# Kernel tuning notes

Hardware: AMD Instinct MI355X
Metric: run time of the kernel (lower is better)

## Reference

```python
import jax, jax.numpy as jnp
import numpy as np

N, E, G = 10000, 40000, 128          # nodes, edges, graphs
NF, EF, H, NH, GD, L = 92, 50, 64, 10, 108, 5  # feat dims, hidden, heads, global dim, layers
EPS = 1e-5

def _lrelu(v):
    return jax.nn.leaky_relu(v, 0.2)

def setup_inputs() -> dict:
    key = jax.random.key(0)
    ks = jax.random.split(key, 24)
    def rn(k, shp, s=0.05):
        return jax.random.normal(k, shp, jnp.float32) * s
    return {
        "x": jax.random.normal(ks[0], (N, NF), jnp.float32),
        "edge_index": jax.random.randint(ks[1], (2, E), 0, N, dtype=jnp.int32),
        "edge_attr": jax.random.normal(ks[2], (E, EF), jnp.float32),
        "batch_idx": jnp.sort(jax.random.randint(ks[3], (N,), 0, G, dtype=jnp.int32)),
        "global_features": jax.random.normal(ks[4], (G, GD), jnp.float32),
        "node_W": rn(ks[5], (NF, H)), "node_b": jnp.zeros((H,), jnp.float32),
        "edge_W": rn(ks[6], (EF, H)), "edge_b": jnp.zeros((H,), jnp.float32),
        "conv_W": rn(ks[7], (L, 2 * H, NH * H)),
        "conv_att": rn(ks[8], (L, NH, 2 * H)),
        "conv_b": jnp.zeros((L, H), jnp.float32),
        "conv_gamma": jnp.ones((L, NH), jnp.float32),
        "conv_beta": jnp.zeros((L, NH), jnp.float32),
        "ga_W1": rn(ks[9], (H + GD, H)), "ga_b1": jnp.zeros((H,), jnp.float32),
        "ga_W2": rn(ks[10], (H, 1)), "ga_b2": jnp.zeros((1,), jnp.float32),
        "out_W1": rn(ks[11], (H, H)), "out_b1": jnp.zeros((H,), jnp.float32),
        "out_W2": rn(ks[12], (H, 1)), "out_b2": jnp.zeros((1,), jnp.float32),
    }

def reference(x, edge_index, edge_attr, batch_idx, global_features,
              node_W, node_b, edge_W, edge_b,
              conv_W, conv_att, conv_b, conv_gamma, conv_beta,
              ga_W1, ga_b1, ga_W2, ga_b2, out_W1, out_b1, out_W2, out_b2):
    row, col = edge_index[0], edge_index[1]
    # embeddings
    h = _lrelu(x @ node_W + node_b)            # [N, H]
    ea = _lrelu(edge_attr @ edge_W + edge_b)   # [E, H]
    initial = h
    inv_std = 1.0 / jnp.sqrt(1.0 + EPS)        # DiffGroupNorm eval: running mean=0, var=1
    for i in range(L):
        xi = jnp.concatenate([h[row], ea], axis=-1)               # [E, 2H]
        xj = jnp.concatenate([h[col], ea], axis=-1)
        hi = _lrelu(xi @ conv_W[i]).reshape(E, NH, H)             # [E, NH, H]
        hj = _lrelu(xj @ conv_W[i]).reshape(E, NH, H)
        alpha = jnp.sum(jnp.concatenate([hi, hj], -1) * conv_att[i][None], -1)  # [E, NH]
        alpha = _lrelu(alpha)
        alpha = alpha * inv_std * conv_gamma[i] + conv_beta[i]
        alpha = jax.nn.softmax(alpha, axis=1)                     # softmax over heads
        msg = (hj * alpha[..., None]).reshape(E, NH * H)
        agg = jax.ops.segment_sum(msg, row, num_segments=N).reshape(N, NH, H)
        h_new = agg.mean(axis=1) + conv_b[i]
        h = h + h_new if i > 0 else h_new
    h = h + initial
    # global attention: softmax over nodes within each graph
    g = global_features[batch_idx]                                 # [N, GD]
    s = _lrelu(jnp.concatenate([h, g], -1) @ ga_W1 + ga_b1)
    score = (s @ ga_W2 + ga_b2)[:, 0]                              # [N]
    smax = jax.ops.segment_max(score, batch_idx, num_segments=G)
    ex = jnp.exp(score - smax[batch_idx])
    denom = jax.ops.segment_sum(ex, batch_idx, num_segments=G)
    w = (ex / denom[batch_idx])[:, None]
    h = h * w
    pooled = jax.ops.segment_sum(h, batch_idx, num_segments=G)     # [G, H]
    out = jax.nn.relu(pooled @ out_W1 + out_b1) @ out_W2 + out_b2
    return out[:, 0]
```

## Files before the change

kernel.cpp:

```cpp
#include <hip/hip_runtime.h>
#include <hip/hip_bf16.h>

#define LRELU(v) ((v) > 0.f ? (v) : 0.2f * (v))

__global__ __launch_bounds__(256) void embed_kernel(
    const float* __restrict__ X, const float* __restrict__ W,
    const float* __restrict__ b, float* __restrict__ out, int M, int K) {
  const int lane = threadIdx.x & 63;
  const int r =
      __builtin_amdgcn_readfirstlane(blockIdx.x * 4 + (threadIdx.x >> 6));
  if (r >= M) return;
  float acc = b[lane];
  const float* Xr = X + (size_t)r * K;
  const float* Wl = W + lane;
  for (int k = 0; k < K; ++k) acc = fmaf(Xr[k], Wl[(size_t)k * 64], acc);
  acc = LRELU(acc);
  out[(size_t)r * 64 + lane] = acc;
}

template <int ROWS>
__global__ __launch_bounds__(256) void gemm_k64_kernel(
    const float* __restrict__ A, const float* __restrict__ W,
    float* __restrict__ C, int M) {
  const int lane = threadIdx.x & 63;
  const int wv =
      __builtin_amdgcn_readfirstlane(blockIdx.x * 4 + (threadIdx.x >> 6));
  const int r0 = wv * ROWS;
  if (r0 >= M) return;
  float acc[ROWS][10];
#pragma unroll
  for (int r = 0; r < ROWS; ++r)
#pragma unroll
    for (int h = 0; h < 10; ++h) acc[r][h] = 0.f;
  const float* Arow = A + (size_t)r0 * 64;
  const float* Wl = W + lane;
  for (int k = 0; k < 64; ++k) {
    float w[10];
#pragma unroll
    for (int h = 0; h < 10; ++h) w[h] = Wl[(size_t)k * 640 + h * 64];
#pragma unroll
    for (int r = 0; r < ROWS; ++r) {
      float a = Arow[r * 64 + k];
#pragma unroll
      for (int h = 0; h < 10; ++h) acc[r][h] = fmaf(a, w[h], acc[r][h]);
    }
  }
#pragma unroll
  for (int r = 0; r < ROWS; ++r) {
    float* Crow = C + (size_t)(r0 + r) * 640;
#pragma unroll
    for (int h = 0; h < 10; ++h) Crow[h * 64 + lane] = acc[r][h];
  }
}

__global__ __launch_bounds__(256) void edge_fused_kernel(
    const float* __restrict__ P, const float* __restrict__ ea,
    const float* __restrict__ Wbot,
    const int* __restrict__ row, const int* __restrict__ col,
    const float* __restrict__ att, const float* __restrict__ gamma,
    const float* __restrict__ beta, float* __restrict__ agg, int E_) {
  const int lane = threadIdx.x & 63;
  const int wv =
      __builtin_amdgcn_readfirstlane(blockIdx.x * 4 + (threadIdx.x >> 6));
  const int e0 = wv * 8;
  if (e0 >= E_) return;

  int eix[8], ris[8], cis[8];
#pragma unroll
  for (int r = 0; r < 8; ++r) {
    int e = (e0 + r < E_) ? (e0 + r) : (E_ - 1);
    eix[r] = e;
    ris[r] = row[e];
    cis[r] = col[e];
  }

  float qacc[8][10];
#pragma unroll
  for (int r = 0; r < 8; ++r)
#pragma unroll
    for (int h = 0; h < 10; ++h) qacc[r][h] = 0.f;

  const float* Wl = Wbot + lane;
  for (int k = 0; k < 64; ++k) {
    float w[10];
#pragma unroll
    for (int h = 0; h < 10; ++h) w[h] = Wl[k * 640 + h * 64];
#pragma unroll
    for (int r = 0; r < 8; ++r) {
      float a = ea[(size_t)eix[r] * 64 + k];
#pragma unroll
      for (int h = 0; h < 10; ++h) qacc[r][h] = fmaf(a, w[h], qacc[r][h]);
    }
  }

  const float inv_std = 0.9999950000374997f;

  float prb[10], pcb[10];
  {
    const float* Pr = P + (size_t)ris[0] * 640 + lane;
    const float* Pc = P + (size_t)cis[0] * 640 + lane;
#pragma unroll
    for (int h = 0; h < 10; ++h) {
      prb[h] = Pr[h * 64];
      pcb[h] = Pc[h * 64];
    }
  }

#pragma unroll
  for (int r = 0; r < 8; ++r) {
    int e = e0 + r;
    if (e >= E_) break;
    float pr[10], pc[10];
#pragma unroll
    for (int h = 0; h < 10; ++h) {
      pr[h] = prb[h];
      pc[h] = pcb[h];
    }
    if (r + 1 < 8) {
      const float* Pr = P + (size_t)ris[r + 1] * 640 + lane;
      const float* Pc = P + (size_t)cis[r + 1] * 640 + lane;
#pragma unroll
      for (int h = 0; h < 10; ++h) {
        prb[h] = Pr[h * 64];
        pcb[h] = Pc[h * 64];
      }
    }
    float hj[10], val[10];
#pragma unroll
    for (int h = 0; h < 10; ++h) {
      float q = qacc[r][h];
      float hi = pr[h] + q;
      float hjv = pc[h] + q;
      hi = LRELU(hi);
      hjv = LRELU(hjv);
      hj[h] = hjv;
      val[h] = fmaf(hi, att[h * 128 + lane], hjv * att[h * 128 + 64 + lane]);
    }
#pragma unroll
    for (int h = 0; h < 10; ++h) {
      float v = val[h];
#pragma unroll
      for (int off = 32; off; off >>= 1) v += __shfl_xor(v, off);
      val[h] = v;
    }
    float mx = -1e30f;
#pragma unroll
    for (int h = 0; h < 10; ++h) {
      float a = val[h];
      a = LRELU(a);
      a = fmaf(a * inv_std, gamma[h], beta[h]);
      val[h] = a;
      mx = fmaxf(mx, a);
    }
    float ssum = 0.f;
#pragma unroll
    for (int h = 0; h < 10; ++h) {
      float ex = __expf(val[h] - mx);
      val[h] = ex;
      ssum += ex;
    }
    float inv = 1.0f / ssum;
    float m = 0.f;
#pragma unroll
    for (int h = 0; h < 10; ++h) m = fmaf(val[h] * inv, hj[h], m);
    atomicAdd(agg + (size_t)ris[r] * 64 + lane, m);
  }
}

__global__ __launch_bounds__(256) void finalize_kernel(
    float* __restrict__ h, float* __restrict__ agg, const float* __restrict__ b,
    const float* __restrict__ h0, int mode, int total) {
  int idx = blockIdx.x * 256 + threadIdx.x;
  if (idx >= total) return;
  int f = idx & 63;
  float v = fmaf(agg[idx], 0.1f, b[f]);
  agg[idx] = 0.f;
  if (mode >= 1) v += h[idx];
  if (mode == 2) v += h0[idx];
  h[idx] = v;
}

__global__ __launch_bounds__(256) void score_kernel(
    const float* __restrict__ h, const int* __restrict__ batch,
    const float* __restrict__ gf, const float* __restrict__ W1,
    const float* __restrict__ b1, const float* __restrict__ W2,
    const float* __restrict__ b2, float* __restrict__ score, int N_) {
  const int lane = threadIdx.x & 63;
  const int n =
      __builtin_amdgcn_readfirstlane(blockIdx.x * 4 + (threadIdx.x >> 6));
  if (n >= N_) return;
  float acc = b1[lane];
  const float* hn = h + (size_t)n * 64;
  const float* W1l = W1 + lane;
#pragma unroll 8
  for (int k = 0; k < 64; ++k) acc = fmaf(hn[k], W1l[k * 64], acc);
  const int bn = batch[n];
  const float* g = gf + (size_t)bn * 108;
#pragma unroll 4
  for (int k = 0; k < 108; ++k) acc = fmaf(g[k], W1l[(64 + k) * 64], acc);
  acc = LRELU(acc);
  float v = acc * W2[lane];
#pragma unroll
  for (int off = 32; off; off >>= 1) v += __shfl_xor(v, off);
  if (lane == 0) score[n] = v + b2[0];
}

__global__ void bounds_kernel(const int* __restrict__ batch,
                              int* __restrict__ start, int N_, int G_) {
  int n = blockIdx.x * blockDim.x + threadIdx.x;
  if (n >= N_) return;
  int b = batch[n];
  int bp = (n == 0) ? -1 : batch[n - 1];
  for (int g = bp + 1; g <= b; ++g) start[g] = n;
  if (n == N_ - 1)
    for (int g = b + 1; g <= G_; ++g) start[g] = N_;
}

__global__ __launch_bounds__(256) void pool_out_kernel(
    const float* __restrict__ h, const float* __restrict__ score,
    const int* __restrict__ start, const float* __restrict__ W1,
    const float* __restrict__ b1, const float* __restrict__ W2,
    const float* __restrict__ b2, float* __restrict__ out) {
  int g = blockIdx.x;
  int s0 = start[g], s1 = start[g + 1];
  int tid = threadIdx.x;
  __shared__ float red[256];
  __shared__ float pool[64];
  __shared__ float sh_smax, sh_denom;
  float lm = -1e30f;
  for (int n = s0 + tid; n < s1; n += 256) lm = fmaxf(lm, score[n]);
  red[tid] = lm;
  __syncthreads();
  for (int off = 128; off; off >>= 1) {
    if (tid < off) red[tid] = fmaxf(red[tid], red[tid + off]);
    __syncthreads();
  }
  if (tid == 0) sh_smax = red[0];
  __syncthreads();
  float smax = sh_smax;
  __syncthreads();
  float ls = 0.f;
  for (int n = s0 + tid; n < s1; n += 256) ls += __expf(score[n] - smax);
  red[tid] = ls;
  __syncthreads();
  for (int off = 128; off; off >>= 1) {
    if (tid < off) red[tid] += red[tid + off];
    __syncthreads();
  }
  if (tid == 0) sh_denom = red[0];
  __syncthreads();
  float denom = sh_denom;
  float invd = denom > 0.f ? 1.0f / denom : 0.f;
  __syncthreads();
  int f = tid & 63, sub = tid >> 6;
  float acc = 0.f;
  for (int n = s0 + sub; n < s1; n += 4)
    acc = fmaf(__expf(score[n] - smax), h[(size_t)n * 64 + f], acc);
  red[tid] = acc;
  __syncthreads();
  if (tid < 64)
    pool[tid] =
        (red[tid] + red[tid + 64] + red[tid + 128] + red[tid + 192]) * invd;
  __syncthreads();
  if (tid < 64) {
    float a = b1[tid];
#pragma unroll 8
    for (int k = 0; k < 64; ++k) a = fmaf(pool[k], W1[k * 64 + tid], a);
    a = fmaxf(a, 0.f);
    red[tid] = a * W2[tid];
  }
  __syncthreads();
  if (tid == 0) {
    float s = 0.f;
    for (int k = 0; k < 64; ++k) s += red[k];
    out[g] = s + b2[0];
  }
}

extern "C" void kernel_launch(void* const* d_in, const int* in_sizes, int n_in,
                              void* d_out, int out_size, void* d_ws,
                              size_t ws_size, hipStream_t stream) {
  const float* x          = (const float*)d_in[0];
  const int*   edge_index = (const int*)d_in[1];
  const float* edge_attr  = (const float*)d_in[2];
  const int*   batch_idx  = (const int*)d_in[3];
  const float* gf         = (const float*)d_in[4];
  const float* node_W     = (const float*)d_in[5];
  const float* node_b     = (const float*)d_in[6];
  const float* edge_W     = (const float*)d_in[7];
  const float* edge_b     = (const float*)d_in[8];
  const float* conv_W     = (const float*)d_in[9];
  const float* conv_att   = (const float*)d_in[10];
  const float* conv_b     = (const float*)d_in[11];
  const float* conv_gamma = (const float*)d_in[12];
  const float* conv_beta  = (const float*)d_in[13];
  const float* ga_W1      = (const float*)d_in[14];
  const float* ga_b1      = (const float*)d_in[15];
  const float* ga_W2      = (const float*)d_in[16];
  const float* ga_b2      = (const float*)d_in[17];
  const float* out_W1     = (const float*)d_in[18];
  const float* out_b1     = (const float*)d_in[19];
  const float* out_W2     = (const float*)d_in[20];
  const float* out_b2     = (const float*)d_in[21];
  float* out = (float*)d_out;

  const int N = in_sizes[3];
  const int E = in_sizes[2] / 50;
  const int G = in_sizes[4] / 108;
  const int L = 5;

  float* ws = (float*)d_ws;
  float* h    = ws;  ws += (size_t)N * 64;
  float* h0   = ws;  ws += (size_t)N * 64;
  float* ea   = ws;  ws += (size_t)E * 64;
  float* P    = ws;  ws += (size_t)N * 640;
  float* agg  = ws;  ws += (size_t)N * 64;
  float* scr  = ws;  ws += N;
  int* gstart = (int*)ws;

  const int* row = edge_index;
  const int* col = edge_index + E;

  embed_kernel<<<(N + 3) / 4, 256, 0, stream>>>(x, node_W, node_b, h0, N, 92);
  embed_kernel<<<(E + 3) / 4, 256, 0, stream>>>(edge_attr, edge_W, edge_b, ea,
                                                E, 50);
  hipMemsetAsync(agg, 0, (size_t)N * 64 * sizeof(float), stream);

  for (int i = 0; i < L; ++i) {
    const float* Wi = conv_W + (size_t)i * 128 * 640;
    gemm_k64_kernel<4><<<(N / 4 + 3) / 4, 256, 0, stream>>>(i == 0 ? h0 : h,
                                                            Wi, P, N);
    int waves = (E + 7) / 8;
    edge_fused_kernel<<<(waves + 3) / 4, 256, 0, stream>>>(
        P, ea, Wi + 64 * 640, row, col, conv_att + (size_t)i * 1280,
        conv_gamma + i * 10, conv_beta + i * 10, agg, E);
    int mode = (i == 0) ? 0 : (i == L - 1 ? 2 : 1);
    finalize_kernel<<<(N * 64 + 255) / 256, 256, 0, stream>>>(
        h, agg, conv_b + i * 64, h0, mode, N * 64);
  }

  score_kernel<<<(N + 3) / 4, 256, 0, stream>>>(h, batch_idx, gf, ga_W1, ga_b1,
                                                ga_W2, ga_b2, scr, N);
  bounds_kernel<<<(N + 255) / 256, 256, 0, stream>>>(batch_idx, gstart, N, G);
  pool_out_kernel<<<G, 256, 0, stream>>>(h, scr, gstart, out_W1, out_b1, out_W2,
                                         out_b2, out);
}
```

Baseline: 780.4 us.

## Fuse finalize into node GEMM, merge embeddings, use DPP wave reductions

Merges the two embedding launches into one kernel. It folds each layer's finalize step (bias, residual, zeroing agg) into the next layer's node GEMM, so only one finalize remains after the loop. The GEMM now takes its A operand from registers through lane shuffles, and both GEMM loops double-buffer the weight loads. Wave reductions use DPP row operations instead of xor shuffles, and occupancy hints are added via launch_bounds. The aim is fewer launches and less global traffic and shuffle latency, at the cost of added register pressure and code complexity.

```diff
diff --git a/kernel.cpp b/kernel.cpp
--- a/kernel.cpp
+++ b/kernel.cpp
@@ -1,14 +1,42 @@
 #include <hip/hip_runtime.h>
-#include <hip/hip_bf16.h>
 
 #define LRELU(v) ((v) > 0.f ? (v) : 0.2f * (v))
 
-__global__ __launch_bounds__(256) void embed_kernel(
-    const float* __restrict__ X, const float* __restrict__ W,
-    const float* __restrict__ b, float* __restrict__ out, int M, int K) {
+template <int CTRL, int RMASK>
+__device__ __forceinline__ float dpp_add(float v) {
+  int moved = __builtin_amdgcn_update_dpp(0, __builtin_bit_cast(int, v), CTRL,
+                                          RMASK, 0xf, true);
+  return v + __builtin_bit_cast(float, moved);
+}
+__device__ __forceinline__ float wave_sum(float v) {
+  v = dpp_add<0x111, 0xf>(v);
+  v = dpp_add<0x112, 0xf>(v);
+  v = dpp_add<0x114, 0xf>(v);
+  v = dpp_add<0x118, 0xf>(v);
+  v = dpp_add<0x142, 0xa>(v);
+  v = dpp_add<0x143, 0xc>(v);
+  return __builtin_bit_cast(
+      float, __builtin_amdgcn_readlane(__builtin_bit_cast(int, v), 63));
+}
+
+__global__ __launch_bounds__(256) void embed2_kernel(
+    const float* __restrict__ x, const float* __restrict__ nW,
+    const float* __restrict__ nb, float* __restrict__ h0, int N_,
+    const float* __restrict__ eattr, const float* __restrict__ eW,
+    const float* __restrict__ eb, float* __restrict__ ea, int E_,
+    int nodeBlocks) {
   const int lane = threadIdx.x & 63;
-  const int r =
-      __builtin_amdgcn_readfirstlane(blockIdx.x * 4 + (threadIdx.x >> 6));
+  const float *X, *W, *b;
+  float* out;
+  int M, K, r;
+  if ((int)blockIdx.x < nodeBlocks) {
+    r = blockIdx.x * 4 + (threadIdx.x >> 6);
+    X = x; W = nW; b = nb; out = h0; M = N_; K = 92;
+  } else {
+    r = (blockIdx.x - nodeBlocks) * 4 + (threadIdx.x >> 6);
+    X = eattr; W = eW; b = eb; out = ea; M = E_; K = 50;
+  }
+  r = __builtin_amdgcn_readfirstlane(r);
   if (r >= M) return;
   float acc = b[lane];
   const float* Xr = X + (size_t)r * K;
@@ -18,42 +46,70 @@
   out[(size_t)r * 64 + lane] = acc;
 }
 
-template <int ROWS>
-__global__ __launch_bounds__(256) void gemm_k64_kernel(
-    const float* __restrict__ A, const float* __restrict__ W,
-    float* __restrict__ C, int M) {
+__global__ __launch_bounds__(256, 4) void update_gemm_kernel(
+    const float* __restrict__ A0, float* __restrict__ h,
+    float* __restrict__ agg, const float* __restrict__ bvec,
+    const float* __restrict__ W, float* __restrict__ P, int M, int mode) {
   const int lane = threadIdx.x & 63;
   const int wv =
       __builtin_amdgcn_readfirstlane(blockIdx.x * 4 + (threadIdx.x >> 6));
-  const int r0 = wv * ROWS;
+  const int r0 = wv * 4;
   if (r0 >= M) return;
-  float acc[ROWS][10];
-#pragma unroll
-  for (int r = 0; r < ROWS; ++r)
-#pragma unroll
-    for (int h = 0; h < 10; ++h) acc[r][h] = 0.f;
-  const float* Arow = A + (size_t)r0 * 64;
+  float hv[4];
+  if (mode < 0) {
+#pragma unroll
+    for (int r = 0; r < 4; ++r) hv[r] = A0[(size_t)(r0 + r) * 64 + lane];
+  } else {
+    float bl = bvec[lane];
+#pragma unroll
+    for (int r = 0; r < 4; ++r) {
+      size_t idx = (size_t)(r0 + r) * 64 + lane;
+      float v = fmaf(agg[idx], 0.1f, bl);
+      if (mode >= 1) v += h[idx];
+      agg[idx] = 0.f;
+      h[idx] = v;
+      hv[r] = v;
+    }
+  }
+  float acc[4][10];
+#pragma unroll
+  for (int r = 0; r < 4; ++r)
+#pragma unroll
+    for (int q = 0; q < 10; ++q) acc[r][q] = 0.f;
   const float* Wl = W + lane;
-  for (int k = 0; k < 64; ++k) {
-    float w[10];
-#pragma unroll
-    for (int h = 0; h < 10; ++h) w[h] = Wl[(size_t)k * 640 + h * 64];
-#pragma unroll
-    for (int r = 0; r < ROWS; ++r) {
-      float a = Arow[r * 64 + k];
-#pragma unroll
-      for (int h = 0; h < 10; ++h) acc[r][h] = fmaf(a, w[h], acc[r][h]);
-    }
-  }
-#pragma unroll
-  for (int r = 0; r < ROWS; ++r) {
-    float* Crow = C + (size_t)(r0 + r) * 640;
-#pragma unroll
-    for (int h = 0; h < 10; ++h) Crow[h * 64 + lane] = acc[r][h];
-  }
-}
-
-__global__ __launch_bounds__(256) void edge_fused_kernel(
+  float wa[10], wb[10];
+#pragma unroll
+  for (int q = 0; q < 10; ++q) wa[q] = Wl[q * 64];
+#pragma unroll 1
+  for (int k = 0; k < 64; k += 2) {
+#pragma unroll
+    for (int q = 0; q < 10; ++q) wb[q] = Wl[(k + 1) * 640 + q * 64];
+#pragma unroll
+    for (int r = 0; r < 4; ++r) {
+      float a = __shfl(hv[r], k);
+#pragma unroll
+      for (int q = 0; q < 10; ++q) acc[r][q] = fmaf(a, wa[q], acc[r][q]);
+    }
+    if (k + 2 < 64) {
+#pragma unroll
+      for (int q = 0; q < 10; ++q) wa[q] = Wl[(k + 2) * 640 + q * 64];
+    }
+#pragma unroll
+    for (int r = 0; r < 4; ++r) {
+      float a = __shfl(hv[r], k + 1);
+#pragma unroll
+      for (int q = 0; q < 10; ++q) acc[r][q] = fmaf(a, wb[q], acc[r][q]);
+    }
+  }
+#pragma unroll
+  for (int r = 0; r < 4; ++r) {
+    float* Crow = P + (size_t)(r0 + r) * 640;
+#pragma unroll
+    for (int q = 0; q < 10; ++q) Crow[q * 64 + lane] = acc[r][q];
+  }
+}
+
+__global__ __launch_bounds__(256, 3) void edge_fused_kernel(
     const float* __restrict__ P, const float* __restrict__ ea,
     const float* __restrict__ Wbot,
     const int* __restrict__ row, const int* __restrict__ col,
@@ -78,106 +134,117 @@
 #pragma unroll
   for (int r = 0; r < 8; ++r)
 #pragma unroll
-    for (int h = 0; h < 10; ++h) qacc[r][h] = 0.f;
+    for (int q = 0; q < 10; ++q) qacc[r][q] = 0.f;
 
   const float* Wl = Wbot + lane;
-  for (int k = 0; k < 64; ++k) {
-    float w[10];
-#pragma unroll
-    for (int h = 0; h < 10; ++h) w[h] = Wl[k * 640 + h * 64];
+  float wa[10], wb[10];
+#pragma unroll
+  for (int q = 0; q < 10; ++q) wa[q] = Wl[q * 64];
+#pragma unroll 1
+  for (int k = 0; k < 64; k += 2) {
+#pragma unroll
+    for (int q = 0; q < 10; ++q) wb[q] = Wl[(k + 1) * 640 + q * 64];
 #pragma unroll
     for (int r = 0; r < 8; ++r) {
       float a = ea[(size_t)eix[r] * 64 + k];
 #pragma unroll
-      for (int h = 0; h < 10; ++h) qacc[r][h] = fmaf(a, w[h], qacc[r][h]);
+      for (int q = 0; q < 10; ++q) qacc[r][q] = fmaf(a, wa[q], qacc[r][q]);
+    }
+    if (k + 2 < 64) {
+#pragma unroll
+      for (int q = 0; q < 10; ++q) wa[q] = Wl[(k + 2) * 640 + q * 64];
+    }
+#pragma unroll
+    for (int r = 0; r < 8; ++r) {
+      float a = ea[(size_t)eix[r] * 64 + k + 1];
+#pragma unroll
+      for (int q = 0; q < 10; ++q) qacc[r][q] = fmaf(a, wb[q], qacc[r][q]);
     }
   }
 
   const float inv_std = 0.9999950000374997f;
+  float gm[10], bt[10];
+#pragma unroll
+  for (int q = 0; q < 10; ++q) {
+    gm[q] = gamma[q];
+    bt[q] = beta[q];
+  }
 
   float prb[10], pcb[10];
   {
     const float* Pr = P + (size_t)ris[0] * 640 + lane;
     const float* Pc = P + (size_t)cis[0] * 640 + lane;
 #pragma unroll
-    for (int h = 0; h < 10; ++h) {
-      prb[h] = Pr[h * 64];
-      pcb[h] = Pc[h * 64];
+    for (int q = 0; q < 10; ++q) {
+      prb[q] = Pr[q * 64];
+      pcb[q] = Pc[q * 64];
     }
   }
 
 #pragma unroll
   for (int r = 0; r < 8; ++r) {
-    int e = e0 + r;
-    if (e >= E_) break;
+    if (e0 + r >= E_) break;
     float pr[10], pc[10];
 #pragma unroll
-    for (int h = 0; h < 10; ++h) {
-      pr[h] = prb[h];
-      pc[h] = pcb[h];
+    for (int q = 0; q < 10; ++q) {
+      pr[q] = prb[q];
+      pc[q] = pcb[q];
     }
     if (r + 1 < 8) {
       const float* Pr = P + (size_t)ris[r + 1] * 640 + lane;
       const float* Pc = P + (size_t)cis[r + 1] * 640 + lane;
 #pragma unroll
-      for (int h = 0; h < 10; ++h) {
-        prb[h] = Pr[h * 64];
-        pcb[h] = Pc[h * 64];
+      for (int q = 0; q < 10; ++q) {
+        prb[q] = Pr[q * 64];
+        pcb[q] = Pc[q * 64];
       }
     }
-    float hj[10], val[10];
-#pragma unroll
-    for (int h = 0; h < 10; ++h) {
-      float q = qacc[r][h];
-      float hi = pr[h] + q;
-      float hjv = pc[h] + q;
+    float hj[10], sv[10];
+#pragma unroll
+    for (int q = 0; q < 10; ++q) {
+      float qc = qacc[r][q];
+      float hi = pr[q] + qc;
+      float hjv = pc[q] + qc;
       hi = LRELU(hi);
       hjv = LRELU(hjv);
-      hj[h] = hjv;
-      val[h] = fmaf(hi, att[h * 128 + lane], hjv * att[h * 128 + 64 + lane]);
-    }
-#pragma unroll
-    for (int h = 0; h < 10; ++h) {
-      float v = val[h];
-#pragma unroll
-      for (int off = 32; off; off >>= 1) v += __shfl_xor(v, off);
-      val[h] = v;
+      hj[q] = hjv;
+      float part =
+          fmaf(hi, att[q * 128 + lane], hjv * att[q * 128 + 64 + lane]);
+      sv[q] = wave_sum(part);
     }
     float mx = -1e30f;
 #pragma unroll
-    for (int h = 0; h < 10; ++h) {
-      float a = val[h];
+    for (int q = 0; q < 10; ++q) {
+      float a = sv[q];
       a = LRELU(a);
-      a = fmaf(a * inv_std, gamma[h], beta[h]);
-      val[h] = a;
+      a = fmaf(a * inv_std, gm[q], bt[q]);
+      sv[q] = a;
       mx = fmaxf(mx, a);
     }
     float ssum = 0.f;
 #pragma unroll
-    for (int h = 0; h < 10; ++h) {
-      float ex = __expf(val[h] - mx);
-      val[h] = ex;
+    for (int q = 0; q < 10; ++q) {
+      float ex = __expf(sv[q] - mx);
+      sv[q] = ex;
       ssum += ex;
     }
     float inv = 1.0f / ssum;
     float m = 0.f;
 #pragma unroll
-    for (int h = 0; h < 10; ++h) m = fmaf(val[h] * inv, hj[h], m);
+    for (int q = 0; q < 10; ++q) m = fmaf(sv[q] * inv, hj[q], m);
     atomicAdd(agg + (size_t)ris[r] * 64 + lane, m);
   }
 }
 
 __global__ __launch_bounds__(256) void finalize_kernel(
     float* __restrict__ h, float* __restrict__ agg, const float* __restrict__ b,
-    const float* __restrict__ h0, int mode, int total) {
+    const float* __restrict__ h0, int total) {
   int idx = blockIdx.x * 256 + threadIdx.x;
   if (idx >= total) return;
   int f = idx & 63;
   float v = fmaf(agg[idx], 0.1f, b[f]);
   agg[idx] = 0.f;
-  if (mode >= 1) v += h[idx];
-  if (mode == 2) v += h0[idx];
-  h[idx] = v;
+  h[idx] = v + h[idx] + h0[idx];
 }
 
 __global__ __launch_bounds__(256) void score_kernel(
@@ -199,9 +266,7 @@
 #pragma unroll 4
   for (int k = 0; k < 108; ++k) acc = fmaf(g[k], W1l[(64 + k) * 64], acc);
   acc = LRELU(acc);
-  float v = acc * W2[lane];
-#pragma unroll
-  for (int off = 32; off; off >>= 1) v += __shfl_xor(v, off);
+  float v = wave_sum(acc * W2[lane]);
   if (lane == 0) score[n] = v + b2[0];
 }
 
@@ -321,23 +386,29 @@
   const int* row = edge_index;
   const int* col = edge_index + E;
 
-  embed_kernel<<<(N + 3) / 4, 256, 0, stream>>>(x, node_W, node_b, h0, N, 92);
-  embed_kernel<<<(E + 3) / 4, 256, 0, stream>>>(edge_attr, edge_W, edge_b, ea,
-                                                E, 50);
-  hipMemsetAsync(agg, 0, (size_t)N * 64 * sizeof(float), stream);
+  int nodeBlocks = (N + 3) / 4;
+  int edgeBlocks = (E + 3) / 4;
+  embed2_kernel<<<nodeBlocks + edgeBlocks, 256, 0, stream>>>(
+      x, node_W, node_b, h0, N, edge_attr, edge_W, edge_b, ea, E, nodeBlocks);
+  (void)hipMemsetAsync(agg, 0, (size_t)N * 64 * sizeof(float), stream);
 
   for (int i = 0; i < L; ++i) {
     const float* Wi = conv_W + (size_t)i * 128 * 640;
-    gemm_k64_kernel<4><<<(N / 4 + 3) / 4, 256, 0, stream>>>(i == 0 ? h0 : h,
-                                                            Wi, P, N);
+    if (i == 0) {
+      update_gemm_kernel<<<(N / 4 + 3) / 4, 256, 0, stream>>>(
+          h0, h, agg, nullptr, Wi, P, N, -1);
+    } else {
+      update_gemm_kernel<<<(N / 4 + 3) / 4, 256, 0, stream>>>(
+          nullptr, h, agg, conv_b + (i - 1) * 64, Wi, P, N,
+          (i - 1) == 0 ? 0 : 1);
+    }
     int waves = (E + 7) / 8;
     edge_fused_kernel<<<(waves + 3) / 4, 256, 0, stream>>>(
         P, ea, Wi + 64 * 640, row, col, conv_att + (size_t)i * 1280,
         conv_gamma + i * 10, conv_beta + i * 10, agg, E);
-    int mode = (i == 0) ? 0 : (i == L - 1 ? 2 : 1);
-    finalize_kernel<<<(N * 64 + 255) / 256, 256, 0, stream>>>(
-        h, agg, conv_b + i * 64, h0, mode, N * 64);
-  }
+  }
+  finalize_kernel<<<(N * 64 + 255) / 256, 256, 0, stream>>>(
+      h, agg, conv_b + (L - 1) * 64, h0, N * 64);
 
   score_kernel<<<(N + 3) / 4, 256, 0, stream>>>(h, batch_idx, gf, ga_W1, ga_b1,
                                                 ga_W2, ga_b2, scr, N);
```

After: 688.6 us. 1.13x faster.
